# Kernel optimization log

Hardware: AMD Instinct MI355X
Metric: run time of the kernel (lower is better)

Reference implementation:

```python
import jax, jax.numpy as jnp
import numpy as np

B, N, D, H = 4096, 64, 32, 64

def setup_inputs() -> dict:
    key = jax.random.key(0)
    ks = jax.random.split(key, 10)
    s = lambda fan_in: 1.0 / np.sqrt(fan_in)
    return {
        "joint_features": jax.random.normal(ks[0], (B, N, D), jnp.float32),
        "Wm1": jax.random.uniform(ks[1], (2 * D, H), jnp.float32, -s(2 * D), s(2 * D)),
        "bm1": jax.random.uniform(ks[2], (H,), jnp.float32, -s(2 * D), s(2 * D)),
        "Wm2": jax.random.uniform(ks[3], (H, D), jnp.float32, -s(H), s(H)),
        "bm2": jax.random.uniform(ks[4], (D,), jnp.float32, -s(H), s(H)),
        "Wu1": jax.random.uniform(ks[5], (2 * D, H), jnp.float32, -s(2 * D), s(2 * D)),
        "bu1": jax.random.uniform(ks[6], (H,), jnp.float32, -s(2 * D), s(2 * D)),
        "Wu2": jax.random.uniform(ks[7], (H, D), jnp.float32, -s(H), s(H)),
        "bu2": jax.random.uniform(ks[8], (D,), jnp.float32, -s(H), s(H)),
        "residual_weight": jnp.float32(0.5),
        "num_joints": N,
    }

def reference(joint_features, Wm1, bm1, Wm2, bm2, Wu1, bu1, Wu2, bu2, residual_weight, num_joints):
    n = num_joints
    # chain topology: directed edges (i->i+1) and (i+1->i); dst receives message
    dst = jnp.concatenate([jnp.arange(n - 1), jnp.arange(1, n)])  # [E]
    src = jnp.concatenate([jnp.arange(1, n), jnp.arange(n - 1)])  # [E]
    # edge gather + concat: [B, E, 2D]
    edge_in = jnp.concatenate([joint_features[:, dst], joint_features[:, src]], axis=-1)
    # message MLP (ReLU after both layers, per original Sequential)
    msg = jax.nn.relu(jax.nn.relu(edge_in @ Wm1 + bm1) @ Wm2 + bm2)  # [B, E, D]
    # scatter-add messages to destination nodes
    messages = jnp.zeros_like(joint_features).at[:, dst].add(msg)  # [B, N, D]
    # per-node update MLP on concat(feature, message)
    upd_in = jnp.concatenate([joint_features, messages], axis=-1)  # [B, N, 2D]
    updated = jax.nn.relu(upd_in @ Wu1 + bu1) @ Wu2 + bu2  # [B, N, D]
    return residual_weight * updated + (1.0 - residual_weight) * joint_features
```

## Files before the change

### kernel.cpp

```cpp
#include <hip/hip_runtime.h>
#include <hip/hip_bf16.h>


typedef __bf16 bf16x8 __attribute__((ext_vector_type(8)));
typedef float  f32x4  __attribute__((ext_vector_type(4)));
typedef unsigned short u16;

#define NBATCH 2
#define ITERS  NBATCH
#define HS  72
#define MBS 40
#define XBS 40

#define SH_OFF   0
#define SMB_OFF  (SH_OFF + 128 * HS)
#define SXB_OFF  (SMB_OFF + 128 * MBS)
#define FB2_OFF  (SXB_OFF + 64 * XBS)
#define FB3_OFF  (FB2_OFF + 4 * 512)
#define FB4_OFF  (FB3_OFF + 8 * 512)
#define BIAS_OFF (FB4_OFF + 4 * 512)
#define SMEM_U16 (BIAS_OFF + 384)

__device__ __forceinline__ u16 f2b(float f) { return __builtin_bit_cast(u16, (__bf16)f); }
__device__ __forceinline__ f32x4 MFMA(bf16x8 a, bf16x8 b, f32x4 c) {
    return __builtin_amdgcn_mfma_f32_16x16x32_bf16(a, b, c, 0, 0, 0);
}
__device__ __forceinline__ bf16x8 pack8(float4 a, float4 b) {
    bf16x8 r = {(__bf16)a.x, (__bf16)a.y, (__bf16)a.z, (__bf16)a.w,
                (__bf16)b.x, (__bf16)b.y, (__bf16)b.z, (__bf16)b.w};
    return r;
}
__device__ __forceinline__ uint2 relu_pack4(f32x4 acc, f32x4 bias) {
    uint2 o;
    o.x = (unsigned)f2b(fmaxf(acc[0] + bias[0], 0.f)) |
          ((unsigned)f2b(fmaxf(acc[1] + bias[1], 0.f)) << 16);
    o.y = (unsigned)f2b(fmaxf(acc[2] + bias[2], 0.f)) |
          ((unsigned)f2b(fmaxf(acc[3] + bias[3], 0.f)) << 16);
    return o;
}
__device__ __forceinline__ void wave_lds_fence() {
    asm volatile("s_waitcnt lgkmcnt(0)" ::: "memory");
}
__device__ __forceinline__ void barrier_lds() {
    asm volatile("s_waitcnt lgkmcnt(0)" ::: "memory");
    __builtin_amdgcn_s_barrier();
    asm volatile("" ::: "memory");
}

__global__ __launch_bounds__(256, 2)
void agn_mfma(const float* __restrict__ x, const float* __restrict__ Wm1,
              const float* __restrict__ bm1, const float* __restrict__ Wm2,
              const float* __restrict__ bm2, const float* __restrict__ Wu1,
              const float* __restrict__ bu1, const float* __restrict__ Wu2,
              const float* __restrict__ bu2, const float* __restrict__ rw_p,
              float* __restrict__ out)
{
    __shared__ __align__(16) u16 smem[SMEM_U16];

    const int t = threadIdx.x;
    const int w = t >> 6;
    const int lane = t & 63;
    const int ln = lane & 15;
    const int q  = lane >> 4;

    float* biasL = (float*)&smem[BIAS_OFF];

    if (t < 64)  { biasL[t] = bm1[t]; biasL[64 + t] = bu1[t]; }
    if (t < 32)  { biasL[128 + t] = bm2[t]; biasL[160 + t] = bu2[t]; }
    if (w == 0) {
#pragma unroll
        for (int ks = 0; ks < 2; ++ks)
#pragma unroll
            for (int ot = 0; ot < 2; ++ot) {
                bf16x8 v;
#pragma unroll
                for (int j = 0; j < 8; ++j)
                    v[j] = (__bf16)Wm2[(ks * 32 + q * 8 + j) * 32 + ot * 16 + ln];
                *(uint4*)&smem[FB2_OFF + (ks * 2 + ot) * 512 + lane * 8] =
                    __builtin_bit_cast(uint4, v);
            }
#pragma unroll
        for (int ks = 0; ks < 2; ++ks)
#pragma unroll
            for (int ht = 0; ht < 4; ++ht) {
                bf16x8 v;
#pragma unroll
                for (int j = 0; j < 8; ++j)
                    v[j] = (__bf16)Wu1[(ks * 32 + q * 8 + j) * 64 + ht * 16 + ln];
                *(uint4*)&smem[FB3_OFF + (ks * 4 + ht) * 512 + lane * 8] =
                    __builtin_bit_cast(uint4, v);
            }
#pragma unroll
        for (int ks = 0; ks < 2; ++ks)
#pragma unroll
            for (int s = 0; s < 2; ++s) {
                bf16x8 v;
#pragma unroll
                for (int j = 0; j < 8; ++j)
                    v[j] = (__bf16)Wu2[(ks * 32 + q * 8 + j) * 32 + s * 16 + ln];
                *(uint4*)&smem[FB4_OFF + (ks * 2 + s) * 512 + lane * 8] =
                    __builtin_bit_cast(uint4, v);
            }
    }

    bf16x8 B1a[4], B1b[4];
#pragma unroll
    for (int nt = 0; nt < 4; ++nt)
#pragma unroll
        for (int j = 0; j < 8; ++j) {
            B1a[nt][j] = (__bf16)Wm1[(q * 8 + j) * 64 + nt * 16 + ln];
            B1b[nt][j] = (__bf16)Wm1[(32 + q * 8 + j) * 64 + nt * 16 + ln];
        }

    const float rw = rw_p[0];
    const float om = 1.f - rw;
    const size_t base = (size_t)blockIdx.x * (NBATCH * 64 * 32);

    for (int it = 0; it < ITERS; ++it) {
        const float* xit = x + base + (size_t)it * (64 * 32);
        float*       oit = out + base + (size_t)it * (64 * 32);

        {
            const int row = t >> 2, ch = t & 3;
            const float* src = xit + row * 32 + ch * 8;
            float4 v0 = *(const float4*)src;
            float4 v1 = *(const float4*)(src + 4);
            *(uint4*)&smem[SXB_OFF + row * XBS + ch * 8] =
                __builtin_bit_cast(uint4, pack8(v0, v1));
        }
        barrier_lds();

#pragma unroll
        for (int m = 0; m < 2; ++m) {
            const int erow = (2 * w + m) * 16 + ln;
            int e = erow;
            if (e >= 126) e = 0;
            const int dst  = (e < 63) ? e : e - 62;
            const int srcn = (e < 63) ? e + 1 : e - 63;
            bf16x8 Ad = __builtin_bit_cast(bf16x8, *(const uint4*)&smem[SXB_OFF + dst * XBS + q * 8]);
            bf16x8 As = __builtin_bit_cast(bf16x8, *(const uint4*)&smem[SXB_OFF + srcn * XBS + q * 8]);
            u16* rowp = &smem[SH_OFF + erow * HS];
#pragma unroll
            for (int ht = 0; ht < 4; ++ht) {
                f32x4 bias = *(const f32x4*)&biasL[ht * 16 + q * 4];
                f32x4 acc = {0.f, 0.f, 0.f, 0.f};
                acc = MFMA(B1a[ht], Ad, acc);
                acc = MFMA(B1b[ht], As, acc);
                *(uint2*)&rowp[ht * 16 + q * 4] = relu_pack4(acc, bias);
            }
        }
        wave_lds_fence();

#pragma unroll
        for (int m = 0; m < 2; ++m) {
            const int row = (2 * w + m) * 16 + ln;
            bf16x8 A0 = __builtin_bit_cast(bf16x8, *(const uint4*)&smem[SH_OFF + row * HS + q * 8]);
            bf16x8 A1 = __builtin_bit_cast(bf16x8, *(const uint4*)&smem[SH_OFF + row * HS + 32 + q * 8]);
#pragma unroll
            for (int s = 0; s < 2; ++s) {
                bf16x8 W0 = __builtin_bit_cast(bf16x8, *(const uint4*)&smem[FB2_OFF + (0 * 2 + s) * 512 + lane * 8]);
                bf16x8 W1 = __builtin_bit_cast(bf16x8, *(const uint4*)&smem[FB2_OFF + (1 * 2 + s) * 512 + lane * 8]);
                f32x4 bias = *(const f32x4*)&biasL[128 + s * 16 + q * 4];
                f32x4 acc = {0.f, 0.f, 0.f, 0.f};
                acc = MFMA(W0, A0, acc);
                acc = MFMA(W1, A1, acc);
                *(uint2*)&smem[SMB_OFF + row * MBS + s * 16 + q * 4] = relu_pack4(acc, bias);
            }
        }
        barrier_lds();

        {
            const int row = w * 16 + ln;
            bf16x8 A0 = __builtin_bit_cast(bf16x8, *(const uint4*)&smem[SXB_OFF + row * XBS + q * 8]);
            float mv[8] = {0.f, 0.f, 0.f, 0.f, 0.f, 0.f, 0.f, 0.f};
            if (row < 63) {
                uint4 u = *(const uint4*)&smem[SMB_OFF + row * MBS + q * 8];
                const unsigned* pu = (const unsigned*)&u;
#pragma unroll
                for (int h = 0; h < 4; ++h) {
                    mv[2 * h]     += __uint_as_float(pu[h] << 16);
                    mv[2 * h + 1] += __uint_as_float(pu[h] & 0xFFFF0000u);
                }
            }
            if (row > 0) {
                uint4 u = *(const uint4*)&smem[SMB_OFF + (62 + row) * MBS + q * 8];
                const unsigned* pu = (const unsigned*)&u;
#pragma unroll
                for (int h = 0; h < 4; ++h) {
                    mv[2 * h]     += __uint_as_float(pu[h] << 16);
                    mv[2 * h + 1] += __uint_as_float(pu[h] & 0xFFFF0000u);
                }
            }
            bf16x8 A1;
#pragma unroll
            for (int j = 0; j < 8; ++j) A1[j] = (__bf16)mv[j];
#pragma unroll
            for (int ht = 0; ht < 4; ++ht) {
                bf16x8 W0 = __builtin_bit_cast(bf16x8, *(const uint4*)&smem[FB3_OFF + (0 * 4 + ht) * 512 + lane * 8]);
                bf16x8 W1 = __builtin_bit_cast(bf16x8, *(const uint4*)&smem[FB3_OFF + (1 * 4 + ht) * 512 + lane * 8]);
                f32x4 bias = *(const f32x4*)&biasL[64 + ht * 16 + q * 4];
                f32x4 acc = {0.f, 0.f, 0.f, 0.f};
                acc = MFMA(W0, A0, acc);
                acc = MFMA(W1, A1, acc);
                *(uint2*)&smem[SH_OFF + row * HS + ht * 16 + q * 4] = relu_pack4(acc, bias);
            }
        }
        wave_lds_fence();

        {
            const int row = w * 16 + ln;
            bf16x8 A0 = __builtin_bit_cast(bf16x8, *(const uint4*)&smem[SH_OFF + row * HS + q * 8]);
            bf16x8 A1 = __builtin_bit_cast(bf16x8, *(const uint4*)&smem[SH_OFF + row * HS + 32 + q * 8]);
#pragma unroll
            for (int s = 0; s < 2; ++s) {
                bf16x8 W0 = __builtin_bit_cast(bf16x8, *(const uint4*)&smem[FB4_OFF + (0 * 2 + s) * 512 + lane * 8]);
                bf16x8 W1 = __builtin_bit_cast(bf16x8, *(const uint4*)&smem[FB4_OFF + (1 * 2 + s) * 512 + lane * 8]);
                f32x4 bias = *(const f32x4*)&biasL[160 + s * 16 + q * 4];
                f32x4 acc = {0.f, 0.f, 0.f, 0.f};
                acc = MFMA(W0, A0, acc);
                acc = MFMA(W1, A1, acc);
                float4 xv = *(const float4*)(xit + row * 32 + s * 16 + q * 4);
                float4 o;
                o.x = rw * (acc[0] + bias[0]) + om * xv.x;
                o.y = rw * (acc[1] + bias[1]) + om * xv.y;
                o.z = rw * (acc[2] + bias[2]) + om * xv.z;
                o.w = rw * (acc[3] + bias[3]) + om * xv.w;
                *(float4*)(oit + row * 32 + s * 16 + q * 4) = o;
            }
        }
        barrier_lds();
    }
}

extern "C" void kernel_launch(void* const* d_in, const int* in_sizes, int n_in,
                              void* d_out, int out_size, void* d_ws, size_t ws_size,
                              hipStream_t stream) {
    const float* x   = (const float*)d_in[0];
    const float* Wm1 = (const float*)d_in[1];
    const float* bm1 = (const float*)d_in[2];
    const float* Wm2 = (const float*)d_in[3];
    const float* bm2 = (const float*)d_in[4];
    const float* Wu1 = (const float*)d_in[5];
    const float* bu1 = (const float*)d_in[6];
    const float* Wu2 = (const float*)d_in[7];
    const float* bu2 = (const float*)d_in[8];
    const float* rw  = (const float*)d_in[9];
    float* out = (float*)d_out;

    const int B = in_sizes[0] / (64 * 32);
    agn_mfma<<<B / NBATCH, 256, 0, stream>>>(x, Wm1, bm1, Wm2, bm2, Wu1, bu1, Wu2, bu2, rw, out);
}
```

Baseline: 118.7 us.

## Prefetch next batch input, spread weight staging across waves, double batches per block

Each block now handles four batch elements instead of two, which halves the grid and amortizes weight staging over more work. Staging of the Wu1 weights is split across waves 1 and 2 instead of all weight staging running on wave 0. The next iteration's input tile is prefetched into registers during the current compute. The residual input loads are issued early and the Wm2 fragments are hoisted out of the row loop. Fewer blocks may reduce occupancy and parallelism across the GPU, and the extra live registers may raise register pressure.

```diff
diff --git a/kernel.cpp b/kernel.cpp
--- a/kernel.cpp
+++ b/kernel.cpp
@@ -6,7 +6,7 @@
 typedef float  f32x4  __attribute__((ext_vector_type(4)));
 typedef unsigned short u16;
 
-#define NBATCH 2
+#define NBATCH 4
 #define ITERS  NBATCH
 #define HS  72
 #define MBS 40
@@ -79,17 +79,18 @@
                 *(uint4*)&smem[FB2_OFF + (ks * 2 + ot) * 512 + lane * 8] =
                     __builtin_bit_cast(uint4, v);
             }
-#pragma unroll
-        for (int ks = 0; ks < 2; ++ks)
-#pragma unroll
-            for (int ht = 0; ht < 4; ++ht) {
-                bf16x8 v;
-#pragma unroll
-                for (int j = 0; j < 8; ++j)
-                    v[j] = (__bf16)Wu1[(ks * 32 + q * 8 + j) * 64 + ht * 16 + ln];
-                *(uint4*)&smem[FB3_OFF + (ks * 4 + ht) * 512 + lane * 8] =
-                    __builtin_bit_cast(uint4, v);
-            }
+    } else if (w == 1 || w == 2) {
+        const int ks = w - 1;
+#pragma unroll
+        for (int ht = 0; ht < 4; ++ht) {
+            bf16x8 v;
+#pragma unroll
+            for (int j = 0; j < 8; ++j)
+                v[j] = (__bf16)Wu1[(ks * 32 + q * 8 + j) * 64 + ht * 16 + ln];
+            *(uint4*)&smem[FB3_OFF + (ks * 4 + ht) * 512 + lane * 8] =
+                __builtin_bit_cast(uint4, v);
+        }
+    } else {
 #pragma unroll
         for (int ks = 0; ks < 2; ++ks)
 #pragma unroll
@@ -116,19 +117,26 @@
     const float om = 1.f - rw;
     const size_t base = (size_t)blockIdx.x * (NBATCH * 64 * 32);
 
+    float4 p0, p1;
+    {
+        const float* xp = x + base + t * 8;
+        p0 = *(const float4*)xp;
+        p1 = *(const float4*)(xp + 4);
+    }
+
     for (int it = 0; it < ITERS; ++it) {
         const float* xit = x + base + (size_t)it * (64 * 32);
         float*       oit = out + base + (size_t)it * (64 * 32);
 
-        {
-            const int row = t >> 2, ch = t & 3;
-            const float* src = xit + row * 32 + ch * 8;
-            float4 v0 = *(const float4*)src;
-            float4 v1 = *(const float4*)(src + 4);
-            *(uint4*)&smem[SXB_OFF + row * XBS + ch * 8] =
-                __builtin_bit_cast(uint4, pack8(v0, v1));
-        }
+        *(uint4*)&smem[SXB_OFF + (t >> 2) * XBS + (t & 3) * 8] =
+            __builtin_bit_cast(uint4, pack8(p0, p1));
         barrier_lds();
+
+        if (it + 1 < ITERS) {
+            const float* xn = xit + 64 * 32 + t * 8;
+            p0 = *(const float4*)xn;
+            p1 = *(const float4*)(xn + 4);
+        }
 
 #pragma unroll
         for (int m = 0; m < 2; ++m) {
@@ -151,26 +159,37 @@
         }
         wave_lds_fence();
 
-#pragma unroll
-        for (int m = 0; m < 2; ++m) {
-            const int row = (2 * w + m) * 16 + ln;
-            bf16x8 A0 = __builtin_bit_cast(bf16x8, *(const uint4*)&smem[SH_OFF + row * HS + q * 8]);
-            bf16x8 A1 = __builtin_bit_cast(bf16x8, *(const uint4*)&smem[SH_OFF + row * HS + 32 + q * 8]);
+        {
+            bf16x8 W2[2][2];
+            f32x4 bb[2];
 #pragma unroll
             for (int s = 0; s < 2; ++s) {
-                bf16x8 W0 = __builtin_bit_cast(bf16x8, *(const uint4*)&smem[FB2_OFF + (0 * 2 + s) * 512 + lane * 8]);
-                bf16x8 W1 = __builtin_bit_cast(bf16x8, *(const uint4*)&smem[FB2_OFF + (1 * 2 + s) * 512 + lane * 8]);
-                f32x4 bias = *(const f32x4*)&biasL[128 + s * 16 + q * 4];
-                f32x4 acc = {0.f, 0.f, 0.f, 0.f};
-                acc = MFMA(W0, A0, acc);
-                acc = MFMA(W1, A1, acc);
-                *(uint2*)&smem[SMB_OFF + row * MBS + s * 16 + q * 4] = relu_pack4(acc, bias);
+                W2[0][s] = __builtin_bit_cast(bf16x8, *(const uint4*)&smem[FB2_OFF + (0 * 2 + s) * 512 + lane * 8]);
+                W2[1][s] = __builtin_bit_cast(bf16x8, *(const uint4*)&smem[FB2_OFF + (1 * 2 + s) * 512 + lane * 8]);
+                bb[s] = *(const f32x4*)&biasL[128 + s * 16 + q * 4];
+            }
+#pragma unroll
+            for (int m = 0; m < 2; ++m) {
+                const int row = (2 * w + m) * 16 + ln;
+                bf16x8 A0 = __builtin_bit_cast(bf16x8, *(const uint4*)&smem[SH_OFF + row * HS + q * 8]);
+                bf16x8 A1 = __builtin_bit_cast(bf16x8, *(const uint4*)&smem[SH_OFF + row * HS + 32 + q * 8]);
+#pragma unroll
+                for (int s = 0; s < 2; ++s) {
+                    f32x4 acc = {0.f, 0.f, 0.f, 0.f};
+                    acc = MFMA(W2[0][s], A0, acc);
+                    acc = MFMA(W2[1][s], A1, acc);
+                    *(uint2*)&smem[SMB_OFF + row * MBS + s * 16 + q * 4] = relu_pack4(acc, bb[s]);
+                }
             }
         }
         barrier_lds();
 
+        const int drow = w * 16 + ln;
+        float4 xv0 = *(const float4*)(xit + drow * 32 + 0 * 16 + q * 4);
+        float4 xv1 = *(const float4*)(xit + drow * 32 + 1 * 16 + q * 4);
+
         {
-            const int row = w * 16 + ln;
+            const int row = drow;
             bf16x8 A0 = __builtin_bit_cast(bf16x8, *(const uint4*)&smem[SXB_OFF + row * XBS + q * 8]);
             float mv[8] = {0.f, 0.f, 0.f, 0.f, 0.f, 0.f, 0.f, 0.f};
             if (row < 63) {
@@ -208,7 +227,7 @@
         wave_lds_fence();
 
         {
-            const int row = w * 16 + ln;
+            const int row = drow;
             bf16x8 A0 = __builtin_bit_cast(bf16x8, *(const uint4*)&smem[SH_OFF + row * HS + q * 8]);
             bf16x8 A1 = __builtin_bit_cast(bf16x8, *(const uint4*)&smem[SH_OFF + row * HS + 32 + q * 8]);
 #pragma unroll
@@ -219,7 +238,7 @@
                 f32x4 acc = {0.f, 0.f, 0.f, 0.f};
                 acc = MFMA(W0, A0, acc);
                 acc = MFMA(W1, A1, acc);
-                float4 xv = *(const float4*)(xit + row * 32 + s * 16 + q * 4);
+                const float4 xv = s ? xv1 : xv0;
                 float4 o;
                 o.x = rw * (acc[0] + bias[0]) + om * xv.x;
                 o.y = rw * (acc[1] + bias[1]) + om * xv.y;
```

Result: faster. 114.9 us (-3.2%).

## Restructure kernel into per-wave node-centric pipeline without block barriers

Applied to the files above, without the earlier changes.

Each wave now owns half of one batch element's nodes and computes the forward and backward edge messages for those nodes directly, summing them in registers. This replaces the edge-indexed layout with its separate scatter step. Second-layer and update weights are hoisted into registers once, x is read straight from global memory instead of being staged in LDS, and per-iteration block barriers become wave-local fences. Each block handles 8 batch elements instead of 2, with two processed concurrently, which cuts launch and weight-setup overhead per element. The costs are higher register pressure, redundant computation of edges at boundary nodes, and more global loads of neighbour rows.

```diff
diff --git a/kernel.cpp b/kernel.cpp
--- a/kernel.cpp
+++ b/kernel.cpp
@@ -6,19 +6,17 @@
 typedef float  f32x4  __attribute__((ext_vector_type(4)));
 typedef unsigned short u16;
 
-#define NBATCH 2
-#define ITERS  NBATCH
-#define HS  72
-#define MBS 40
-#define XBS 40
-
+#define NBATCH 8
+#define ITERS (NBATCH / 2)
+#define HS 72
+#define MS 40
+
+#define FB2_OFF 0
+#define FB3_OFF (FB2_OFF + 4 * 512)
+#define FB4_OFF (FB3_OFF + 8 * 512)
 #define SH_OFF   0
-#define SMB_OFF  (SH_OFF + 128 * HS)
-#define SXB_OFF  (SMB_OFF + 128 * MBS)
-#define FB2_OFF  (SXB_OFF + 64 * XBS)
-#define FB3_OFF  (FB2_OFF + 4 * 512)
-#define FB4_OFF  (FB3_OFF + 8 * 512)
-#define BIAS_OFF (FB4_OFF + 4 * 512)
+#define SM_OFF   (SH_OFF + 256 * HS)
+#define BIAS_OFF (SM_OFF + 128 * MS)
 #define SMEM_U16 (BIAS_OFF + 384)
 
 __device__ __forceinline__ u16 f2b(float f) { return __builtin_bit_cast(u16, (__bf16)f); }
@@ -62,6 +60,8 @@
     const int lane = t & 63;
     const int ln = lane & 15;
     const int q  = lane >> 4;
+    const int bl = w >> 1;
+    const int g0 = (w & 1) * 32;
 
     float* biasL = (float*)&smem[BIAS_OFF];
 
@@ -71,25 +71,26 @@
 #pragma unroll
         for (int ks = 0; ks < 2; ++ks)
 #pragma unroll
-            for (int ot = 0; ot < 2; ++ot) {
+            for (int s = 0; s < 2; ++s) {
                 bf16x8 v;
 #pragma unroll
                 for (int j = 0; j < 8; ++j)
-                    v[j] = (__bf16)Wm2[(ks * 32 + q * 8 + j) * 32 + ot * 16 + ln];
-                *(uint4*)&smem[FB2_OFF + (ks * 2 + ot) * 512 + lane * 8] =
+                    v[j] = (__bf16)Wm2[(ks * 32 + q * 8 + j) * 32 + s * 16 + ln];
+                *(uint4*)&smem[FB2_OFF + (ks * 2 + s) * 512 + lane * 8] =
                     __builtin_bit_cast(uint4, v);
             }
-#pragma unroll
-        for (int ks = 0; ks < 2; ++ks)
-#pragma unroll
-            for (int ht = 0; ht < 4; ++ht) {
-                bf16x8 v;
-#pragma unroll
-                for (int j = 0; j < 8; ++j)
-                    v[j] = (__bf16)Wu1[(ks * 32 + q * 8 + j) * 64 + ht * 16 + ln];
-                *(uint4*)&smem[FB3_OFF + (ks * 4 + ht) * 512 + lane * 8] =
-                    __builtin_bit_cast(uint4, v);
-            }
+    } else if (w == 1 || w == 2) {
+        const int ks = w - 1;
+#pragma unroll
+        for (int ht = 0; ht < 4; ++ht) {
+            bf16x8 v;
+#pragma unroll
+            for (int j = 0; j < 8; ++j)
+                v[j] = (__bf16)Wu1[(ks * 32 + q * 8 + j) * 64 + ht * 16 + ln];
+            *(uint4*)&smem[FB3_OFF + (ks * 4 + ht) * 512 + lane * 8] =
+                __builtin_bit_cast(uint4, v);
+        }
+    } else {
 #pragma unroll
         for (int ks = 0; ks < 2; ++ks)
 #pragma unroll
@@ -112,123 +113,132 @@
             B1b[nt][j] = (__bf16)Wm1[(32 + q * 8 + j) * 64 + nt * 16 + ln];
         }
 
+    barrier_lds();
+
+    bf16x8 W2[2][2], W3[2][4], W4[2][2];
+#pragma unroll
+    for (int ks = 0; ks < 2; ++ks) {
+#pragma unroll
+        for (int s = 0; s < 2; ++s) {
+            W2[ks][s] = __builtin_bit_cast(bf16x8, *(const uint4*)&smem[FB2_OFF + (ks * 2 + s) * 512 + lane * 8]);
+            W4[ks][s] = __builtin_bit_cast(bf16x8, *(const uint4*)&smem[FB4_OFF + (ks * 2 + s) * 512 + lane * 8]);
+        }
+#pragma unroll
+        for (int ht = 0; ht < 4; ++ht)
+            W3[ks][ht] = __builtin_bit_cast(bf16x8, *(const uint4*)&smem[FB3_OFF + (ks * 4 + ht) * 512 + lane * 8]);
+    }
+    barrier_lds();
+
     const float rw = rw_p[0];
     const float om = 1.f - rw;
     const size_t base = (size_t)blockIdx.x * (NBATCH * 64 * 32);
 
     for (int it = 0; it < ITERS; ++it) {
-        const float* xit = x + base + (size_t)it * (64 * 32);
-        float*       oit = out + base + (size_t)it * (64 * 32);
-
-        {
-            const int row = t >> 2, ch = t & 3;
-            const float* src = xit + row * 32 + ch * 8;
-            float4 v0 = *(const float4*)src;
-            float4 v1 = *(const float4*)(src + 4);
-            *(uint4*)&smem[SXB_OFF + row * XBS + ch * 8] =
-                __builtin_bit_cast(uint4, pack8(v0, v1));
-        }
-        barrier_lds();
-
-#pragma unroll
-        for (int m = 0; m < 2; ++m) {
-            const int erow = (2 * w + m) * 16 + ln;
-            int e = erow;
-            if (e >= 126) e = 0;
-            const int dst  = (e < 63) ? e : e - 62;
-            const int srcn = (e < 63) ? e + 1 : e - 63;
-            bf16x8 Ad = __builtin_bit_cast(bf16x8, *(const uint4*)&smem[SXB_OFF + dst * XBS + q * 8]);
-            bf16x8 As = __builtin_bit_cast(bf16x8, *(const uint4*)&smem[SXB_OFF + srcn * XBS + q * 8]);
-            u16* rowp = &smem[SH_OFF + erow * HS];
+        const float* xb = x + base + (size_t)(it * 2 + bl) * (64 * 32);
+        float*       ob = out + base + (size_t)(it * 2 + bl) * (64 * 32);
+
+        bf16x8 Xd[2];
+
+#pragma unroll
+        for (int nt = 0; nt < 2; ++nt) {
+            const int n = g0 + nt * 16 + ln;
+            const float* pd = xb + n * 32 + q * 8;
+            float4 d0 = *(const float4*)pd, d1 = *(const float4*)(pd + 4);
+            Xd[nt] = pack8(d0, d1);
+            const int nn = (n == 63) ? n : n + 1;
+            const int np = (n == 0)  ? n : n - 1;
+            const float* pn = xb + nn * 32 + q * 8;
+            const float* pp = xb + np * 32 + q * 8;
+            float4 a0 = *(const float4*)pn, a1 = *(const float4*)(pn + 4);
+            float4 b0 = *(const float4*)pp, b1 = *(const float4*)(pp + 4);
+            bf16x8 Xn = pack8(a0, a1);
+            bf16x8 Xp = pack8(b0, b1);
+            u16* rf = &smem[SH_OFF + (w * 64 + nt * 16 + ln) * HS];
+            u16* rb = &smem[SH_OFF + (w * 64 + 32 + nt * 16 + ln) * HS];
 #pragma unroll
             for (int ht = 0; ht < 4; ++ht) {
                 f32x4 bias = *(const f32x4*)&biasL[ht * 16 + q * 4];
-                f32x4 acc = {0.f, 0.f, 0.f, 0.f};
-                acc = MFMA(B1a[ht], Ad, acc);
-                acc = MFMA(B1b[ht], As, acc);
-                *(uint2*)&rowp[ht * 16 + q * 4] = relu_pack4(acc, bias);
-            }
-        }
-        wave_lds_fence();
-
-#pragma unroll
-        for (int m = 0; m < 2; ++m) {
-            const int row = (2 * w + m) * 16 + ln;
-            bf16x8 A0 = __builtin_bit_cast(bf16x8, *(const uint4*)&smem[SH_OFF + row * HS + q * 8]);
-            bf16x8 A1 = __builtin_bit_cast(bf16x8, *(const uint4*)&smem[SH_OFF + row * HS + 32 + q * 8]);
-#pragma unroll
-            for (int s = 0; s < 2; ++s) {
-                bf16x8 W0 = __builtin_bit_cast(bf16x8, *(const uint4*)&smem[FB2_OFF + (0 * 2 + s) * 512 + lane * 8]);
-                bf16x8 W1 = __builtin_bit_cast(bf16x8, *(const uint4*)&smem[FB2_OFF + (1 * 2 + s) * 512 + lane * 8]);
+                f32x4 af = {0.f, 0.f, 0.f, 0.f};
+                af = MFMA(B1a[ht], Xd[nt], af);
+                af = MFMA(B1b[ht], Xn, af);
+                *(uint2*)&rf[ht * 16 + q * 4] = relu_pack4(af, bias);
+                f32x4 ab = {0.f, 0.f, 0.f, 0.f};
+                ab = MFMA(B1a[ht], Xd[nt], ab);
+                ab = MFMA(B1b[ht], Xp, ab);
+                *(uint2*)&rb[ht * 16 + q * 4] = relu_pack4(ab, bias);
+            }
+        }
+        wave_lds_fence();
+
+#pragma unroll
+        for (int nt = 0; nt < 2; ++nt) {
+            const int n = g0 + nt * 16 + ln;
+            const u16* rf = &smem[SH_OFF + (w * 64 + nt * 16 + ln) * HS];
+            const u16* rb = &smem[SH_OFF + (w * 64 + 32 + nt * 16 + ln) * HS];
+            bf16x8 hf0 = __builtin_bit_cast(bf16x8, *(const uint4*)&rf[q * 8]);
+            bf16x8 hf1 = __builtin_bit_cast(bf16x8, *(const uint4*)&rf[32 + q * 8]);
+            bf16x8 hb0 = __builtin_bit_cast(bf16x8, *(const uint4*)&rb[q * 8]);
+            bf16x8 hb1 = __builtin_bit_cast(bf16x8, *(const uint4*)&rb[32 + q * 8]);
+#pragma unroll
+            for (int s = 0; s < 2; ++s) {
                 f32x4 bias = *(const f32x4*)&biasL[128 + s * 16 + q * 4];
-                f32x4 acc = {0.f, 0.f, 0.f, 0.f};
-                acc = MFMA(W0, A0, acc);
-                acc = MFMA(W1, A1, acc);
-                *(uint2*)&smem[SMB_OFF + row * MBS + s * 16 + q * 4] = relu_pack4(acc, bias);
-            }
-        }
-        barrier_lds();
-
-        {
-            const int row = w * 16 + ln;
-            bf16x8 A0 = __builtin_bit_cast(bf16x8, *(const uint4*)&smem[SXB_OFF + row * XBS + q * 8]);
-            float mv[8] = {0.f, 0.f, 0.f, 0.f, 0.f, 0.f, 0.f, 0.f};
-            if (row < 63) {
-                uint4 u = *(const uint4*)&smem[SMB_OFF + row * MBS + q * 8];
-                const unsigned* pu = (const unsigned*)&u;
-#pragma unroll
-                for (int h = 0; h < 4; ++h) {
-                    mv[2 * h]     += __uint_as_float(pu[h] << 16);
-                    mv[2 * h + 1] += __uint_as_float(pu[h] & 0xFFFF0000u);
+                f32x4 cf = {0.f, 0.f, 0.f, 0.f};
+                f32x4 cb = {0.f, 0.f, 0.f, 0.f};
+                cf = MFMA(W2[0][s], hf0, cf); cf = MFMA(W2[1][s], hf1, cf);
+                cb = MFMA(W2[0][s], hb0, cb); cb = MFMA(W2[1][s], hb1, cb);
+                float m4[4];
+#pragma unroll
+                for (int r = 0; r < 4; ++r) {
+                    float vf = (n != 63) ? fmaxf(cf[r] + bias[r], 0.f) : 0.f;
+                    float vb = (n != 0)  ? fmaxf(cb[r] + bias[r], 0.f) : 0.f;
+                    m4[r] = vf + vb;
                 }
-            }
-            if (row > 0) {
-                uint4 u = *(const uint4*)&smem[SMB_OFF + (62 + row) * MBS + q * 8];
-                const unsigned* pu = (const unsigned*)&u;
-#pragma unroll
-                for (int h = 0; h < 4; ++h) {
-                    mv[2 * h]     += __uint_as_float(pu[h] << 16);
-                    mv[2 * h + 1] += __uint_as_float(pu[h] & 0xFFFF0000u);
-                }
-            }
-            bf16x8 A1;
-#pragma unroll
-            for (int j = 0; j < 8; ++j) A1[j] = (__bf16)mv[j];
+                uint2 o;
+                o.x = (unsigned)f2b(m4[0]) | ((unsigned)f2b(m4[1]) << 16);
+                o.y = (unsigned)f2b(m4[2]) | ((unsigned)f2b(m4[3]) << 16);
+                *(uint2*)&smem[SM_OFF + (bl * 64 + n) * MS + s * 16 + q * 4] = o;
+            }
+        }
+        wave_lds_fence();
+
+#pragma unroll
+        for (int nt = 0; nt < 2; ++nt) {
+            const int n = g0 + nt * 16 + ln;
+            bf16x8 A1 = __builtin_bit_cast(bf16x8, *(const uint4*)&smem[SM_OFF + (bl * 64 + n) * MS + q * 8]);
+            u16* rh = &smem[SH_OFF + (w * 64 + nt * 16 + ln) * HS];
 #pragma unroll
             for (int ht = 0; ht < 4; ++ht) {
-                bf16x8 W0 = __builtin_bit_cast(bf16x8, *(const uint4*)&smem[FB3_OFF + (0 * 4 + ht) * 512 + lane * 8]);
-                bf16x8 W1 = __builtin_bit_cast(bf16x8, *(const uint4*)&smem[FB3_OFF + (1 * 4 + ht) * 512 + lane * 8]);
                 f32x4 bias = *(const f32x4*)&biasL[64 + ht * 16 + q * 4];
                 f32x4 acc = {0.f, 0.f, 0.f, 0.f};
-                acc = MFMA(W0, A0, acc);
-                acc = MFMA(W1, A1, acc);
-                *(uint2*)&smem[SH_OFF + row * HS + ht * 16 + q * 4] = relu_pack4(acc, bias);
-            }
-        }
-        wave_lds_fence();
-
-        {
-            const int row = w * 16 + ln;
-            bf16x8 A0 = __builtin_bit_cast(bf16x8, *(const uint4*)&smem[SH_OFF + row * HS + q * 8]);
-            bf16x8 A1 = __builtin_bit_cast(bf16x8, *(const uint4*)&smem[SH_OFF + row * HS + 32 + q * 8]);
-#pragma unroll
-            for (int s = 0; s < 2; ++s) {
-                bf16x8 W0 = __builtin_bit_cast(bf16x8, *(const uint4*)&smem[FB4_OFF + (0 * 2 + s) * 512 + lane * 8]);
-                bf16x8 W1 = __builtin_bit_cast(bf16x8, *(const uint4*)&smem[FB4_OFF + (1 * 2 + s) * 512 + lane * 8]);
+                acc = MFMA(W3[0][ht], Xd[nt], acc);
+                acc = MFMA(W3[1][ht], A1, acc);
+                *(uint2*)&rh[ht * 16 + q * 4] = relu_pack4(acc, bias);
+            }
+        }
+        wave_lds_fence();
+
+#pragma unroll
+        for (int nt = 0; nt < 2; ++nt) {
+            const int n = g0 + nt * 16 + ln;
+            const u16* rh = &smem[SH_OFF + (w * 64 + nt * 16 + ln) * HS];
+            bf16x8 A0 = __builtin_bit_cast(bf16x8, *(const uint4*)&rh[q * 8]);
+            bf16x8 A1 = __builtin_bit_cast(bf16x8, *(const uint4*)&rh[32 + q * 8]);
+#pragma unroll
+            for (int s = 0; s < 2; ++s) {
                 f32x4 bias = *(const f32x4*)&biasL[160 + s * 16 + q * 4];
                 f32x4 acc = {0.f, 0.f, 0.f, 0.f};
-                acc = MFMA(W0, A0, acc);
-                acc = MFMA(W1, A1, acc);
-                float4 xv = *(const float4*)(xit + row * 32 + s * 16 + q * 4);
+                acc = MFMA(W4[0][s], A0, acc);
+                acc = MFMA(W4[1][s], A1, acc);
+                float4 xv = *(const float4*)(xb + n * 32 + s * 16 + q * 4);
                 float4 o;
                 o.x = rw * (acc[0] + bias[0]) + om * xv.x;
                 o.y = rw * (acc[1] + bias[1]) + om * xv.y;
                 o.z = rw * (acc[2] + bias[2]) + om * xv.z;
                 o.w = rw * (acc[3] + bias[3]) + om * xv.w;
-                *(float4*)(oit + row * 32 + s * 16 + q * 4) = o;
-            }
-        }
-        barrier_lds();
+                *(float4*)(ob + n * 32 + s * 16 + q * 4) = o;
+            }
+        }
+        wave_lds_fence();
     }
 }
 
```

After: 120.2 us. No clear change (+1.3%).
